# Kernel tuning notes

Hardware: AMD Instinct MI355X
Metric: run time of the kernel (lower is better)

The kernel has to match this reference:

```python
import jax, jax.numpy as jnp
import numpy as np

B, T, D = 512, 200, 512

def setup_inputs() -> dict:
    key = jax.random.key(0)
    k1, k2, k3 = jax.random.split(key, 3)
    inputs = jax.random.normal(k1, (B, T, D), dtype=jnp.float32)
    # Keras 'uniform' initializer -> U(-0.05, 0.05)
    W = jax.random.uniform(k2, (T, T), minval=-0.05, maxval=0.05, dtype=jnp.float32)
    b = jax.random.uniform(k3, (T,), minval=-0.05, maxval=0.05, dtype=jnp.float32)
    return {"inputs": inputs, "W": W, "b": b}

def reference(inputs, W, b):
    # x = permute(inputs, (0,2,1)) -> [B, D, T]; scores over timestep axis
    # a = softmax(tanh(x @ W + b)) along last axis (T)
    scores = jnp.tanh(jnp.einsum('btd,ts->bds', inputs, W) + b)  # [B, D, T]
    a = jax.nn.softmax(scores, axis=-1)                           # softmax over T
    # permute back to [B, T, D], elementwise multiply, sum over T -> [B, D]
    out = jnp.einsum('bdt,btd->bd', a, inputs)
    return out
```

## Files before the change

### kernel.cpp

```cpp
#include <hip/hip_runtime.h>
#include <cstdint>
#include <cstddef>

#define B_DIM 512
#define T_DIM 200
#define D_DIM 512
#define NPAD  208
#define NKG   28
#define NT    13
#define KS_STEPS 7
#define SLICE 3208

typedef short  short8  __attribute__((ext_vector_type(8)));
typedef float  floatx4 __attribute__((ext_vector_type(4)));

__device__ __forceinline__ unsigned short f2bf(float f) {
  unsigned int u = __float_as_uint(f);
  u += 0x7fffu + ((u >> 16) & 1u);
  return (unsigned short)(u >> 16);
}
__device__ __forceinline__ float bf2f(unsigned short h) {
  return __uint_as_float(((unsigned int)h) << 16);
}

__global__ void prep_w_kernel(const float* __restrict__ W,
                              unsigned short* __restrict__ wf) {
  int idx = blockIdx.x * blockDim.x + threadIdx.x;
  if (idx >= NKG * 8 * NPAD) return;
  int k = idx / NPAD;
  int n = idx - k * NPAD;
  float v = (k < T_DIM && n < T_DIM) ? W[k * T_DIM + n] : 0.0f;
  wf[((size_t)(k >> 3) * NPAD + n) * 8 + (k & 7)] = f2bf(v);
}

__global__ __launch_bounds__(256, 4)
void attn_kernel(const float* __restrict__ X,
                 const unsigned short* __restrict__ wf,
                 const float* __restrict__ bias,
                 float* __restrict__ out) {
  __shared__ __align__(16) unsigned short Xa[4 * SLICE];

  const int tid  = threadIdx.x;
  const int wv   = tid >> 6;
  const int lane = tid & 63;
  const int l15  = lane & 15;
  const int g    = lane >> 4;

  const int bid  = blockIdx.x;
  const int bb   = bid >> 3;
  const int dblk = (bid & 7) << 6;
  const int d0   = dblk + (wv << 4);

  {
    const float* xb = X + (size_t)bb * (T_DIM * D_DIM) + dblk;
    #pragma unroll
    for (int it = 0; it < 13; ++it) {
      int i = it * 256 + tid;
      if (i < 3200) {
        int t  = i >> 4;
        int c4 = i & 15;
        float4 v = *(const float4*)(xb + (size_t)t * D_DIM + (c4 << 2));
        unsigned short* dst = Xa + (c4 >> 2) * SLICE
                            + ((t >> 3) * 16 + ((c4 & 3) << 2)) * 8 + (t & 7);
        dst[0]  = f2bf(v.x);
        dst[8]  = f2bf(v.y);
        dst[16] = f2bf(v.z);
        dst[24] = f2bf(v.w);
      }
    }
  }
  __syncthreads();

  unsigned short* Xw = Xa + wv * SLICE;

  floatx4 acc[NT];
  #pragma unroll
  for (int nt = 0; nt < NT; ++nt)
    acc[nt] = (floatx4){0.f, 0.f, 0.f, 0.f};

  #pragma unroll
  for (int ks = 0; ks < KS_STEPS; ++ks) {
    const int kg = ks * 4 + g;
    short8 a = (short8){0, 0, 0, 0, 0, 0, 0, 0};
    if (ks < 6 || g == 0)
      a = *(const short8*)&Xw[(kg * 16 + l15) * 8];
    const unsigned short* wp = wf + ((size_t)kg * NPAD + l15) * 8;
    #pragma unroll
    for (int nt = 0; nt < NT; ++nt) {
      short8 bfr = *(const short8*)(wp + nt * 16 * 8);
      acc[nt] = __builtin_amdgcn_mfma_f32_16x16x32_bf16(a, bfr, acc[nt], 0, 0, 0);
    }
  }

  float part[4] = {0.f, 0.f, 0.f, 0.f};
  float rs[4]   = {0.f, 0.f, 0.f, 0.f};
  #pragma unroll
  for (int nt = 0; nt < NT; ++nt) {
    const int t = nt * 16 + l15;
    const bool valid = (t < T_DIM);
    const float bvn = valid ? bias[t] : 0.0f;
    const unsigned short* xp = &Xw[((t >> 3) * 16) * 8 + (t & 7)];
    #pragma unroll
    for (int r = 0; r < 4; ++r) {
      if (valid) {
        float z  = acc[nt][r] + bvn;
        float e  = __expf(2.0f * z);
        float th = 1.0f - __fdividef(2.0f, e + 1.0f);
        float p  = __expf(th);
        rs[r]   += p;
        const int m = g * 4 + r;
        part[r] += p * bf2f(xp[m * 8]);
      }
    }
  }
  #pragma unroll
  for (int off = 1; off <= 8; off <<= 1)
    #pragma unroll
    for (int r = 0; r < 4; ++r) {
      part[r] += __shfl_xor(part[r], off, 16);
      rs[r]   += __shfl_xor(rs[r],   off, 16);
    }

  if (l15 == 0) {
    #pragma unroll
    for (int r = 0; r < 4; ++r)
      out[(size_t)bb * D_DIM + d0 + g * 4 + r] = part[r] * __frcp_rn(rs[r]);
  }
}

extern "C" void kernel_launch(void* const* d_in, const int* in_sizes, int n_in,
                              void* d_out, int out_size, void* d_ws, size_t ws_size,
                              hipStream_t stream) {
  const float* X  = (const float*)d_in[0];
  const float* W  = (const float*)d_in[1];
  const float* bs = (const float*)d_in[2];
  float* out = (float*)d_out;
  unsigned short* wf = (unsigned short*)d_ws;

  const int wtot = NKG * 8 * NPAD;
  hipLaunchKernelGGL(prep_w_kernel, dim3((wtot + 255) / 256), dim3(256), 0, stream,
                     W, wf);
  hipLaunchKernelGGL(attn_kernel, dim3(4096), dim3(256), 0, stream,
                     X, wf, bs, out);
}
```

Measured before the change: 337.6 us.

## Software-pipeline W fragment loads across MFMAs and streamline epilogue conversions

Flattens the k-step/n-tile MFMA loop into a 91-fragment sequence. An 8-deep register ring buffer prefetches the global W fragments ahead of their use, and the next X fragment is read from LDS mid-step, so memory latency overlaps with MFMA work. It also replaces the software float-to-bf16 rounding with the packed hardware convert instruction. The epilogue's tail-tile bounds check is peeled out of the hot loop. The cost is more register pressure from the prefetch buffers, which could reduce occupancy under launch_bounds(256,4).

```diff
diff --git a/kernel.cpp b/kernel.cpp
--- a/kernel.cpp
+++ b/kernel.cpp
@@ -9,6 +9,8 @@
 #define NKG   28
 #define NT    13
 #define KS_STEPS 7
+#define NFRAG 91
+#define PIPE  8
 #define SLICE 3208
 
 typedef short  short8  __attribute__((ext_vector_type(8)));
@@ -21,6 +23,11 @@
 }
 __device__ __forceinline__ float bf2f(unsigned short h) {
   return __uint_as_float(((unsigned int)h) << 16);
+}
+__device__ __forceinline__ unsigned int cvt_pk_bf16(float a, float b) {
+  unsigned int d;
+  asm("v_cvt_pk_bf16_f32 %0, %1, %2" : "=v"(d) : "v"(a), "v"(b));
+  return d;
 }
 
 __global__ void prep_w_kernel(const float* __restrict__ W,
@@ -56,61 +63,91 @@
     #pragma unroll
     for (int it = 0; it < 13; ++it) {
       int i = it * 256 + tid;
-      if (i < 3200) {
+      if (it < 12 || tid < 128) {
         int t  = i >> 4;
         int c4 = i & 15;
         float4 v = *(const float4*)(xb + (size_t)t * D_DIM + (c4 << 2));
         unsigned short* dst = Xa + (c4 >> 2) * SLICE
                             + ((t >> 3) * 16 + ((c4 & 3) << 2)) * 8 + (t & 7);
-        dst[0]  = f2bf(v.x);
-        dst[8]  = f2bf(v.y);
-        dst[16] = f2bf(v.z);
-        dst[24] = f2bf(v.w);
+        unsigned int w01 = cvt_pk_bf16(v.x, v.y);
+        unsigned int w23 = cvt_pk_bf16(v.z, v.w);
+        dst[0]  = (unsigned short)(w01 & 0xffffu);
+        dst[8]  = (unsigned short)(w01 >> 16);
+        dst[16] = (unsigned short)(w23 & 0xffffu);
+        dst[24] = (unsigned short)(w23 >> 16);
       }
     }
   }
   __syncthreads();
 
   unsigned short* Xw = Xa + wv * SLICE;
+  const unsigned short* wl = wf + (size_t)l15 * 8;
 
   floatx4 acc[NT];
   #pragma unroll
   for (int nt = 0; nt < NT; ++nt)
     acc[nt] = (floatx4){0.f, 0.f, 0.f, 0.f};
 
+#define BLOADF(dst, f) do {                                                  \
+    const int _ks = (f) / NT, _nt = (f) % NT;                                \
+    (dst) = *(const short8*)(wl + ((size_t)(_ks * 4 + g) * NPAD + _nt * 16) * 8); \
+  } while (0)
+
+  short8 buf[PIPE];
+  short8 a_cur, a_nxt;
+
+  a_cur = *(const short8*)&Xw[((g * 16) + l15) * 8];
   #pragma unroll
-  for (int ks = 0; ks < KS_STEPS; ++ks) {
-    const int kg = ks * 4 + g;
-    short8 a = (short8){0, 0, 0, 0, 0, 0, 0, 0};
-    if (ks < 6 || g == 0)
-      a = *(const short8*)&Xw[(kg * 16 + l15) * 8];
-    const unsigned short* wp = wf + ((size_t)kg * NPAD + l15) * 8;
-    #pragma unroll
-    for (int nt = 0; nt < NT; ++nt) {
-      short8 bfr = *(const short8*)(wp + nt * 16 * 8);
-      acc[nt] = __builtin_amdgcn_mfma_f32_16x16x32_bf16(a, bfr, acc[nt], 0, 0, 0);
+  for (int f = 0; f < PIPE; ++f) BLOADF(buf[f], f);
+
+  #pragma unroll
+  for (int f = 0; f < NFRAG; ++f) {
+    const int nt   = f % NT;
+    const int ks   = f / NT;
+    const int slot = f % PIPE;
+    acc[nt] = __builtin_amdgcn_mfma_f32_16x16x32_bf16(a_cur, buf[slot], acc[nt], 0, 0, 0);
+    if (f + PIPE < NFRAG) BLOADF(buf[slot], f + PIPE);
+    if (nt == 6 && ks < 6) {
+      const int kgn = (ks + 1) * 4 + g;
+      if (ks < 5 || g == 0)
+        a_nxt = *(const short8*)&Xw[((kgn * 16) + l15) * 8];
+      else
+        a_nxt = (short8){0, 0, 0, 0, 0, 0, 0, 0};
     }
+    if (nt == NT - 1) a_cur = a_nxt;
   }
+#undef BLOADF
 
   float part[4] = {0.f, 0.f, 0.f, 0.f};
   float rs[4]   = {0.f, 0.f, 0.f, 0.f};
   #pragma unroll
-  for (int nt = 0; nt < NT; ++nt) {
+  for (int nt = 0; nt < 12; ++nt) {
     const int t = nt * 16 + l15;
-    const bool valid = (t < T_DIM);
-    const float bvn = valid ? bias[t] : 0.0f;
+    const float bvn = bias[t];
     const unsigned short* xp = &Xw[((t >> 3) * 16) * 8 + (t & 7)];
     #pragma unroll
     for (int r = 0; r < 4; ++r) {
-      if (valid) {
-        float z  = acc[nt][r] + bvn;
-        float e  = __expf(2.0f * z);
-        float th = 1.0f - __fdividef(2.0f, e + 1.0f);
-        float p  = __expf(th);
-        rs[r]   += p;
-        const int m = g * 4 + r;
-        part[r] += p * bf2f(xp[m * 8]);
-      }
+      float z  = acc[nt][r] + bvn;
+      float e  = __expf(2.0f * z);
+      float th = 1.0f - __fdividef(2.0f, e + 1.0f);
+      float p  = __expf(th);
+      rs[r]   += p;
+      part[r] += p * bf2f(xp[(g * 4 + r) * 8]);
+    }
+  }
+  {
+    const bool valid = (l15 < 8);
+    const int tc = valid ? (192 + l15) : 199;
+    const float bvn = bias[tc];
+    const unsigned short* xp = &Xw[((tc >> 3) * 16) * 8 + (tc & 7)];
+    #pragma unroll
+    for (int r = 0; r < 4; ++r) {
+      float z  = acc[12][r] + bvn;
+      float e  = __expf(2.0f * z);
+      float th = 1.0f - __fdividef(2.0f, e + 1.0f);
+      float p  = valid ? __expf(th) : 0.0f;
+      rs[r]   += p;
+      part[r] += p * bf2f(xp[(g * 4 + r) * 8]);
     }
   }
   #pragma unroll
```

Result: faster. 329.8 us (-2.3%).

## Split N-tiles across waves with 32-column blocks and cross-wave softmax combine

Applied to the files above, without the earlier changes.

Each block now handles 32 d-columns instead of 64, and the grid doubles. The four waves split the 13 N-tiles of the T dimension among themselves instead of each wave covering all 13 tiles for its own 16 columns. Partial softmax numerators and denominators are combined across waves through shared memory, and B/A fragments are software-prefetched one k-step ahead. Packed bf16 conversion replaces the manual rounding. The aim is to cut per-wave accumulator registers and LDS size to raise occupancy and overlap loads with MFMA, at the cost of an extra barrier, a shared-memory reduction, and W fragments being reloaded by more blocks.

```diff
diff --git a/kernel.cpp b/kernel.cpp
--- a/kernel.cpp
+++ b/kernel.cpp
@@ -22,6 +22,11 @@
 __device__ __forceinline__ float bf2f(unsigned short h) {
   return __uint_as_float(((unsigned int)h) << 16);
 }
+__device__ __forceinline__ unsigned int cvt_pk_bf16(float a, float b) {
+  unsigned int d;
+  asm("v_cvt_pk_bf16_f32 %0, %1, %2" : "=v"(d) : "v"(a), "v"(b));
+  return d;
+}
 
 __global__ void prep_w_kernel(const float* __restrict__ W,
                               unsigned short* __restrict__ wf) {
@@ -38,7 +43,8 @@
                  const unsigned short* __restrict__ wf,
                  const float* __restrict__ bias,
                  float* __restrict__ out) {
-  __shared__ __align__(16) unsigned short Xa[4 * SLICE];
+  __shared__ __align__(16) unsigned short Xs[2 * SLICE];
+  __shared__ __align__(16) float comb[4][32][2];
 
   const int tid  = threadIdx.x;
   const int wv   = tid >> 6;
@@ -47,84 +53,140 @@
   const int g    = lane >> 4;
 
   const int bid  = blockIdx.x;
-  const int bb   = bid >> 3;
-  const int dblk = (bid & 7) << 6;
-  const int d0   = dblk + (wv << 4);
+  const int bb   = bid >> 4;
+  const int dblk = (bid & 15) << 5;
 
   {
     const float* xb = X + (size_t)bb * (T_DIM * D_DIM) + dblk;
     #pragma unroll
-    for (int it = 0; it < 13; ++it) {
+    for (int it = 0; it < 7; ++it) {
       int i = it * 256 + tid;
-      if (i < 3200) {
-        int t  = i >> 4;
-        int c4 = i & 15;
+      if (it < 6 || tid < 64) {
+        int t  = i >> 3;
+        int c4 = i & 7;
         float4 v = *(const float4*)(xb + (size_t)t * D_DIM + (c4 << 2));
-        unsigned short* dst = Xa + (c4 >> 2) * SLICE
+        unsigned short* dst = Xs + (c4 >> 2) * SLICE
                             + ((t >> 3) * 16 + ((c4 & 3) << 2)) * 8 + (t & 7);
-        dst[0]  = f2bf(v.x);
-        dst[8]  = f2bf(v.y);
-        dst[16] = f2bf(v.z);
-        dst[24] = f2bf(v.w);
+        unsigned int w01 = cvt_pk_bf16(v.x, v.y);
+        unsigned int w23 = cvt_pk_bf16(v.z, v.w);
+        dst[0]  = (unsigned short)(w01 & 0xffffu);
+        dst[8]  = (unsigned short)(w01 >> 16);
+        dst[16] = (unsigned short)(w23 & 0xffffu);
+        dst[24] = (unsigned short)(w23 >> 16);
       }
     }
   }
   __syncthreads();
 
-  unsigned short* Xw = Xa + wv * SLICE;
-
-  floatx4 acc[NT];
-  #pragma unroll
-  for (int nt = 0; nt < NT; ++nt)
-    acc[nt] = (floatx4){0.f, 0.f, 0.f, 0.f};
+  const int nt0 = (wv == 0) ? 0 : (1 + 3 * wv);
+  const int ntw = (wv == 0) ? 4 : 3;
+
+  floatx4 acc[2][4];
+  #pragma unroll
+  for (int h = 0; h < 2; ++h)
+    #pragma unroll
+    for (int j = 0; j < 4; ++j)
+      acc[h][j] = (floatx4){0.f, 0.f, 0.f, 0.f};
+
+  const unsigned short* wk = wf + ((size_t)g * NPAD + nt0 * 16 + l15) * 8;
+
+  short8 bc[4], bn[4];
+  short8 a0c, a1c, a0n, a1n;
+
+  #pragma unroll
+  for (int j = 0; j < 4; ++j)
+    if (j < ntw) bc[j] = *(const short8*)(wk + j * 128);
+  a0c = *(const short8*)&Xs[(g * 16 + l15) * 8];
+  a1c = *(const short8*)&Xs[SLICE + (g * 16 + l15) * 8];
 
   #pragma unroll
   for (int ks = 0; ks < KS_STEPS; ++ks) {
-    const int kg = ks * 4 + g;
-    short8 a = (short8){0, 0, 0, 0, 0, 0, 0, 0};
-    if (ks < 6 || g == 0)
-      a = *(const short8*)&Xw[(kg * 16 + l15) * 8];
-    const unsigned short* wp = wf + ((size_t)kg * NPAD + l15) * 8;
-    #pragma unroll
-    for (int nt = 0; nt < NT; ++nt) {
-      short8 bfr = *(const short8*)(wp + nt * 16 * 8);
-      acc[nt] = __builtin_amdgcn_mfma_f32_16x16x32_bf16(a, bfr, acc[nt], 0, 0, 0);
-    }
-  }
-
-  float part[4] = {0.f, 0.f, 0.f, 0.f};
-  float rs[4]   = {0.f, 0.f, 0.f, 0.f};
-  #pragma unroll
-  for (int nt = 0; nt < NT; ++nt) {
-    const int t = nt * 16 + l15;
-    const bool valid = (t < T_DIM);
-    const float bvn = valid ? bias[t] : 0.0f;
-    const unsigned short* xp = &Xw[((t >> 3) * 16) * 8 + (t & 7)];
-    #pragma unroll
-    for (int r = 0; r < 4; ++r) {
-      if (valid) {
-        float z  = acc[nt][r] + bvn;
-        float e  = __expf(2.0f * z);
-        float th = 1.0f - __fdividef(2.0f, e + 1.0f);
-        float p  = __expf(th);
-        rs[r]   += p;
+    if (ks < 6) {
+      const unsigned short* wkn = wk + (size_t)(ks + 1) * (4 * NPAD * 8);
+      #pragma unroll
+      for (int j = 0; j < 4; ++j)
+        if (j < ntw) bn[j] = *(const short8*)(wkn + j * 128);
+      const int kgn = (ks + 1) * 4 + g;
+      if (ks < 5 || g == 0) {
+        a0n = *(const short8*)&Xs[(kgn * 16 + l15) * 8];
+        a1n = *(const short8*)&Xs[SLICE + (kgn * 16 + l15) * 8];
+      } else {
+        a0n = (short8){0, 0, 0, 0, 0, 0, 0, 0};
+        a1n = (short8){0, 0, 0, 0, 0, 0, 0, 0};
+      }
+    }
+    #pragma unroll
+    for (int j = 0; j < 4; ++j)
+      if (j < ntw) {
+        acc[0][j] = __builtin_amdgcn_mfma_f32_16x16x32_bf16(a0c, bc[j], acc[0][j], 0, 0, 0);
+        acc[1][j] = __builtin_amdgcn_mfma_f32_16x16x32_bf16(a1c, bc[j], acc[1][j], 0, 0, 0);
+      }
+    if (ks < 6) {
+      a0c = a0n; a1c = a1n;
+      #pragma unroll
+      for (int j = 0; j < 4; ++j) bc[j] = bn[j];
+    }
+  }
+
+  float part[2][4], rs[2][4];
+  #pragma unroll
+  for (int h = 0; h < 2; ++h)
+    #pragma unroll
+    for (int r = 0; r < 4; ++r) { part[h][r] = 0.f; rs[h][r] = 0.f; }
+
+  #pragma unroll
+  for (int j = 0; j < 4; ++j) {
+    if (j < ntw) {
+      const int nt = nt0 + j;
+      const int t  = nt * 16 + l15;
+      const bool valid = (t < T_DIM);
+      const int tc = valid ? t : (T_DIM - 1);
+      const float bvn = bias[tc];
+      const unsigned short* xp = &Xs[((tc >> 3) * 16) * 8 + (tc & 7)];
+      #pragma unroll
+      for (int r = 0; r < 4; ++r) {
         const int m = g * 4 + r;
-        part[r] += p * bf2f(xp[m * 8]);
+        #pragma unroll
+        for (int h = 0; h < 2; ++h) {
+          float z  = acc[h][j][r] + bvn;
+          float e  = __expf(2.0f * z);
+          float th = 1.0f - __fdividef(2.0f, e + 1.0f);
+          float p  = valid ? __expf(th) : 0.0f;
+          rs[h][r]   += p;
+          part[h][r] += p * bf2f(xp[h * SLICE + m * 8]);
+        }
       }
     }
   }
   #pragma unroll
   for (int off = 1; off <= 8; off <<= 1)
     #pragma unroll
-    for (int r = 0; r < 4; ++r) {
-      part[r] += __shfl_xor(part[r], off, 16);
-      rs[r]   += __shfl_xor(rs[r],   off, 16);
-    }
+    for (int h = 0; h < 2; ++h)
+      #pragma unroll
+      for (int r = 0; r < 4; ++r) {
+        part[h][r] += __shfl_xor(part[h][r], off, 16);
+        rs[h][r]   += __shfl_xor(rs[h][r],   off, 16);
+      }
 
   if (l15 == 0) {
     #pragma unroll
-    for (int r = 0; r < 4; ++r)
-      out[(size_t)bb * D_DIM + d0 + g * 4 + r] = part[r] * __frcp_rn(rs[r]);
+    for (int h = 0; h < 2; ++h)
+      #pragma unroll
+      for (int r = 0; r < 4; ++r) {
+        comb[wv][h * 16 + g * 4 + r][0] = part[h][r];
+        comb[wv][h * 16 + g * 4 + r][1] = rs[h][r];
+      }
+  }
+  __syncthreads();
+
+  if (tid < 32) {
+    float ps = 0.f, ss = 0.f;
+    #pragma unroll
+    for (int w = 0; w < 4; ++w) {
+      ps += comb[w][tid][0];
+      ss += comb[w][tid][1];
+    }
+    out[(size_t)bb * D_DIM + dblk + tid] = ps * __frcp_rn(ss);
   }
 }
 
@@ -140,6 +202,6 @@
   const int wtot = NKG * 8 * NPAD;
   hipLaunchKernelGGL(prep_w_kernel, dim3((wtot + 255) / 256), dim3(256), 0, stream,
                      W, wf);
-  hipLaunchKernelGGL(attn_kernel, dim3(4096), dim3(256), 0, stream,
+  hipLaunchKernelGGL(attn_kernel, dim3(8192), dim3(256), 0, stream,
                      X, wf, bs, out);
 }
```

Measured after the change: 319.6 us. 5.3% less time.
